# Performance work log

Hardware: AMD Instinct MI355X
Metric: run time of the kernel (lower is better)

The kernel has to match this reference:

```python
import jax, jax.numpy as jnp
import numpy as np

B, S, D, H = 4, 2048, 1024, 16
HD = D // H  # head_dim = 64


def setup_inputs() -> dict:
    key = jax.random.key(0)
    kx, kq, kk, kv, ko = jax.random.split(key, 5)
    scale = 1.0 / np.sqrt(D)
    return {
        "x": jax.random.normal(kx, (B, S, D), dtype=jnp.float32),
        "wq": jax.random.normal(kq, (D, D), dtype=jnp.float32) * scale,
        "wk": jax.random.normal(kk, (D, D), dtype=jnp.float32) * scale,
        "wv": jax.random.normal(kv, (D, D), dtype=jnp.float32) * scale,
        "wo": jax.random.normal(ko, (D, D), dtype=jnp.float32) * scale,
    }


def reference(x, wq, wk, wv, wo):
    b, s, d = x.shape
    # nn.Linear stores weight [out, in]: y = x @ W.T
    q = (x @ wq.T).reshape(b, s, H, HD)
    k = (x @ wk.T).reshape(b, s, H, HD)
    v = (x @ wv.T).reshape(b, s, H, HD)
    # scores: [b, h, s, s]
    scores = jnp.einsum("bqhd,bkhd->bhqk", q, k) / np.sqrt(HD)
    causal = jnp.triu(jnp.ones((s, s), dtype=bool), k=1)
    scores = jnp.where(causal, -jnp.inf, scores)
    attn = jax.nn.softmax(scores, axis=-1)
    out = jnp.einsum("bhqk,bkhd->bqhd", attn, v).reshape(b, s, d)
    return out @ wo.T
```

## Files before the change

### kernel.cpp

```cpp
#include <hip/hip_runtime.h>
#include <math.h>

typedef unsigned short u16;
typedef __attribute__((ext_vector_type(8))) short short8;
typedef __attribute__((ext_vector_type(4))) short short4v;
typedef __attribute__((ext_vector_type(4))) float f32x4;
typedef __attribute__((ext_vector_type(2))) unsigned int uint2v;
typedef __attribute__((ext_vector_type(4))) unsigned int uint4v;

constexpr int Bn = 4, Sn = 2048, Dn = 1024, Hn = 16;
constexpr float SCL = 0.125f * 1.44269504f;

__device__ __forceinline__ u16 f2bf(float f) {
  unsigned u = __float_as_uint(f);
  u += 0x7fffu + ((u >> 16) & 1u);
  return (u16)(u >> 16);
}

__device__ __forceinline__ f32x4 mfma32(short8 a, short8 b, f32x4 c) {
  return __builtin_amdgcn_mfma_f32_16x16x32_bf16(a, b, c, 0, 0, 0);
}

__device__ __forceinline__ void gl_lds16(const u16* g, u16* l) {
  __builtin_amdgcn_global_load_lds(
      (const __attribute__((address_space(1))) unsigned int*)g,
      (__attribute__((address_space(3))) unsigned int*)l, 16, 0, 0);
}

__global__ __launch_bounds__(256) void cast_all(
    const float4* __restrict__ x, const float4* __restrict__ wq,
    const float4* __restrict__ wk, const float4* __restrict__ wv,
    const float4* __restrict__ wo, ushort4* __restrict__ xb,
    ushort4* __restrict__ wqb, ushort4* __restrict__ wkb,
    ushort4* __restrict__ wvb, ushort4* __restrict__ wob) {
  const int blk = blockIdx.x;
  const float4* in;
  ushort4* out;
  int base;
  float s = 1.0f;
  if (blk < 8192) {
    in = x; out = xb; base = blk;
  } else if (blk < 9216) {
    in = wq; out = wqb; base = blk - 8192; s = SCL;
  } else if (blk < 10240) {
    in = wk; out = wkb; base = blk - 9216;
  } else if (blk < 11264) {
    in = wv; out = wvb; base = blk - 10240;
  } else {
    in = wo; out = wob; base = blk - 11264;
  }
  const int i = base * 256 + threadIdx.x;
  const float4 f = in[i];
  ushort4 o;
  o.x = f2bf(f.x * s); o.y = f2bf(f.y * s);
  o.z = f2bf(f.z * s); o.w = f2bf(f.w * s);
  out[i] = o;
}

template <int MODE>
__device__ __forceinline__ void gemm_body(const u16* __restrict__ A,
                                          const u16* __restrict__ W,
                                          u16* __restrict__ Cb,
                                          float* __restrict__ Cf,
                                          int bx, int by,
                                          u16* __restrict__ Asm,
                                          u16* __restrict__ Wsm) {
  const int t = threadIdx.x;
  const int w = t >> 6, l = t & 63;
  const int wy = w >> 1, wx = w & 1;
  const int q = l >> 4, r = l & 15;
  const int m0 = bx * 128, n0 = by * 128;

  f32x4 acc[4][4] = {};

  for (int k0 = 0; k0 < 1024; k0 += 64) {
    __syncthreads();
#pragma unroll
    for (int i = 0; i < 4; ++i) {
      const int c = t + i * 256;
      const int row = c >> 3, cl = c & 7;
      const int cg = cl ^ (row & 7);
      gl_lds16(A + (size_t)(m0 + row) * 1024 + k0 + cg * 8, &Asm[c * 8]);
      gl_lds16(W + (size_t)(n0 + row) * 1024 + k0 + cg * 8, &Wsm[c * 8]);
    }
    __syncthreads();
#pragma unroll
    for (int kf = 0; kf < 2; ++kf) {
      short8 af[4], bf[4];
#pragma unroll
      for (int mi = 0; mi < 4; ++mi) {
        const int rowA = wy * 64 + mi * 16 + r;
        af[mi] = *(const short8*)&Asm[rowA * 64 + ((kf * 4 + q) ^ (rowA & 7)) * 8];
        const int rowB = wx * 64 + mi * 16 + r;
        bf[mi] = *(const short8*)&Wsm[rowB * 64 + ((kf * 4 + q) ^ (rowB & 7)) * 8];
      }
#pragma unroll
      for (int mi = 0; mi < 4; ++mi)
#pragma unroll
        for (int ni = 0; ni < 4; ++ni)
          acc[mi][ni] = mfma32(af[mi], bf[ni], acc[mi][ni]);
    }
  }

  if (MODE == 2) {
    const int bq = m0 >> 11;
    const int jt = ((m0 & 2047) >> 6) + wy;
    const int hh = (n0 >> 6) + wx;
    u16* vt_t = Cb + ((size_t)((bq * 16 + hh) * 32) + jt) * 4096;
#pragma unroll
    for (int mi = 0; mi < 4; ++mi)
#pragma unroll
      for (int ni = 0; ni < 4; ++ni) {
        short4v pk;
#pragma unroll
        for (int e = 0; e < 4; ++e) pk[e] = (short)f2bf(acc[mi][ni][e]);
        const int hd = ni * 16 + r;
        const int c2 = q + 4 * (mi >> 1);
        *(short4v*)&vt_t[hd * 64 + ((c2 ^ (r & 7)) * 8) + (mi & 1) * 4] = pk;
      }
    return;
  }

#pragma unroll
  for (int mi = 0; mi < 4; ++mi) {
    const int row = m0 + wy * 64 + mi * 16 + q * 4;
#pragma unroll
    for (int ni = 0; ni < 4; ++ni) {
      const int col = n0 + wx * 64 + ni * 16 + r;
#pragma unroll
      for (int e = 0; e < 4; ++e) {
        if (MODE == 1)
          Cf[(size_t)(row + e) * 1024 + col] = acc[mi][ni][e];
        else
          Cb[(size_t)(row + e) * 1024 + col] = f2bf(acc[mi][ni][e]);
      }
    }
  }
}

__global__ __launch_bounds__(256) void gemm_qkv(const u16* __restrict__ A,
                                                const u16* __restrict__ Wq,
                                                const u16* __restrict__ Wk,
                                                const u16* __restrict__ Wv,
                                                u16* __restrict__ Cq,
                                                u16* __restrict__ Ck,
                                                u16* __restrict__ Vt) {
  __shared__ u16 Asm[128 * 64];
  __shared__ u16 Wsm[128 * 64];
  const int z = blockIdx.z;
  if (z == 2)
    gemm_body<2>(A, Wv, Vt, nullptr, blockIdx.x, blockIdx.y, Asm, Wsm);
  else
    gemm_body<0>(A, z ? Wk : Wq, z ? Ck : Cq, nullptr, blockIdx.x, blockIdx.y,
                 Asm, Wsm);
}

__global__ __launch_bounds__(256) void gemm_out(const u16* __restrict__ A,
                                                const u16* __restrict__ W,
                                                float* __restrict__ C) {
  __shared__ u16 Asm[128 * 64];
  __shared__ u16 Wsm[128 * 64];
  gemm_body<1>(A, W, nullptr, C, blockIdx.x, blockIdx.y, Asm, Wsm);
}

__global__ __launch_bounds__(128) void attn_v10(const u16* __restrict__ Qb,
                                                const u16* __restrict__ Kb,
                                                const u16* __restrict__ Vt,
                                                u16* __restrict__ Ob) {
  const int i = blockIdx.x;
  const int st = 31 - (i >> 6);
  const int grp = (i & 7) + 8 * ((i >> 3) & 7);
  const int b = grp >> 4, h = grp & 15;
  const int t = threadIdx.x;
  const int w = t >> 6, l = t & 63;
  const int q = l >> 4, r = l & 15;

  __shared__ u16 Kd[2][4096];
  __shared__ u16 Vd[4096];

  const size_t kgbase = (size_t)(b * Sn) * Dn + h * 64;
  const size_t vgbase = (size_t)((b * Hn + h) * 32) * 4096;

  const u16* kg[4];
  const u16* vg[4];
#pragma unroll
  for (int ii = 0; ii < 4; ++ii) {
    const int c = t + ii * 128, row = c >> 3, cl = c & 7;
    kg[ii] = Kb + kgbase + (size_t)row * Dn + (cl ^ (row & 7)) * 8;
    vg[ii] = Vt + vgbase + c * 8;
  }
  const int rx = r & 7;
  const int b0 = r * 64 + ((q ^ rx) * 8);
  const int b1 = r * 64 + (((4 + q) ^ rx) * 8);

  const int qb64 = st * 64;

  short8 Qf[2][2];
#pragma unroll
  for (int mi = 0; mi < 2; ++mi)
#pragma unroll
    for (int kf = 0; kf < 2; ++kf)
      Qf[mi][kf] = *(const short8*)(Qb +
          (size_t)(b * Sn + qb64 + w * 32 + mi * 16 + r) * Dn + h * 64 +
          kf * 32 + q * 8);

  f32x4 O[2][4] = {};
  float l_[2] = {0.f, 0.f};

#pragma unroll
  for (int ii = 0; ii < 4; ++ii)
    gl_lds16(kg[ii], &Kd[0][(t + ii * 128) * 8]);

  const u16* kgt[4];
  const u16* vgt[4];
#pragma unroll
  for (int ii = 0; ii < 4; ++ii) {
    kgt[ii] = kg[ii] + 64 * Dn;
    vgt[ii] = vg[ii];
  }

  for (int jt = 0; jt <= st; ++jt) {
    __syncthreads();

#pragma unroll
    for (int ii = 0; ii < 4; ++ii) {
      gl_lds16(vgt[ii], &Vd[(t + ii * 128) * 8]);
      vgt[ii] += 4096;
    }
    if (jt < st) {
      u16* kl = &Kd[(jt + 1) & 1][0];
#pragma unroll
      for (int ii = 0; ii < 4; ++ii) {
        gl_lds16(kgt[ii], kl + (t + ii * 128) * 8);
        kgt[ii] += 64 * Dn;
      }
    }

    const u16* KtA = &Kd[jt & 1][b0];
    const u16* KtB = &Kd[jt & 1][b1];

    short8 Kf[4][2];
#pragma unroll
    for (int ni = 0; ni < 4; ++ni) {
      Kf[ni][0] = *(const short8*)(KtA + ni * 1024);
      Kf[ni][1] = *(const short8*)(KtB + ni * 1024);
    }

    f32x4 S[2][4] = {};
    __builtin_amdgcn_s_setprio(1);
#pragma unroll
    for (int ni = 0; ni < 4; ++ni)
#pragma unroll
      for (int kf = 0; kf < 2; ++kf) {
        S[0][ni] = mfma32(Kf[ni][kf], Qf[0][kf], S[0][ni]);
        S[1][ni] = mfma32(Kf[ni][kf], Qf[1][kf], S[1][ni]);
      }
    __builtin_amdgcn_s_setprio(0);

    if (jt == st) {
#pragma unroll
      for (int mi = 0; mi < 2; ++mi) {
        const int qrow = w * 32 + mi * 16 + r;
#pragma unroll
        for (int ni = 0; ni < 4; ++ni) {
          const int key = ni * 16 + q * 4;
#pragma unroll
          for (int e = 0; e < 4; ++e)
            if (key + e > qrow) S[mi][ni][e] = -3.0e38f;
        }
      }
    }

    short8 P8[2][2];
#pragma unroll
    for (int mi = 0; mi < 2; ++mi)
#pragma unroll
      for (int np = 0; np < 2; ++np) {
        unsigned pw[4];
#pragma unroll
        for (int half = 0; half < 2; ++half) {
          const int ni = 2 * np + half;
          const float p0 = __builtin_amdgcn_exp2f(S[mi][ni][0]);
          const float p1 = __builtin_amdgcn_exp2f(S[mi][ni][1]);
          const float p2 = __builtin_amdgcn_exp2f(S[mi][ni][2]);
          const float p3 = __builtin_amdgcn_exp2f(S[mi][ni][3]);
          l_[mi] += (p0 + p1) + (p2 + p3);
          unsigned plo, phi;
          asm("v_cvt_pk_bf16_f32 %0, %1, %2" : "=v"(plo) : "v"(p0), "v"(p1));
          asm("v_cvt_pk_bf16_f32 %0, %1, %2" : "=v"(phi) : "v"(p2), "v"(p3));
          pw[half * 2] = plo;
          pw[half * 2 + 1] = phi;
        }
        const uint4v pk4 = {pw[0], pw[1], pw[2], pw[3]};
        P8[mi][np] = __builtin_bit_cast(short8, pk4);
      }

    if (jt < st)
      asm volatile("s_waitcnt vmcnt(4)" ::: "memory");
    else
      asm volatile("s_waitcnt vmcnt(0)" ::: "memory");
    __builtin_amdgcn_s_barrier();
    __builtin_amdgcn_sched_barrier(0);

    __builtin_amdgcn_s_setprio(1);
#pragma unroll
    for (int np = 0; np < 2; ++np) {
      const int vb = np ? b1 : b0;
#pragma unroll
      for (int ni2 = 0; ni2 < 4; ++ni2) {
        const short8 vvx = *(const short8*)(&Vd[vb + ni2 * 1024]);
        O[0][ni2] = mfma32(vvx, P8[0][np], O[0][ni2]);
        O[1][ni2] = mfma32(vvx, P8[1][np], O[1][ni2]);
      }
    }
    __builtin_amdgcn_s_setprio(0);
  }

#pragma unroll
  for (int mi = 0; mi < 2; ++mi) {
    float s = l_[mi];
    s += __shfl_xor(s, 16, 64);
    s += __shfl_xor(s, 32, 64);
    const float rl = __builtin_amdgcn_rcpf(s);
#pragma unroll
    for (int ni2 = 0; ni2 < 4; ++ni2) {
      short4v o;
#pragma unroll
      for (int e = 0; e < 4; ++e) o[e] = (short)f2bf(O[mi][ni2][e] * rl);
      *(short4v*)(Ob + (size_t)(b * Sn + qb64 + w * 32 + mi * 16 + r) * Dn +
                  h * 64 + ni2 * 16 + q * 4) = o;
    }
  }
}

extern "C" void kernel_launch(void* const* d_in, const int* in_sizes, int n_in,
                              void* d_out, int out_size, void* d_ws, size_t ws_size,
                              hipStream_t stream) {
  const float* x  = (const float*)d_in[0];
  const float* wq = (const float*)d_in[1];
  const float* wk = (const float*)d_in[2];
  const float* wv = (const float*)d_in[3];
  const float* wo = (const float*)d_in[4];
  float* out = (float*)d_out;

  u16* xb  = (u16*)d_ws;
  u16* wqb = xb + 8388608;
  u16* wkb = wqb + 1048576;
  u16* wvb = wkb + 1048576;
  u16* wob = wvb + 1048576;
  u16* qb  = wob + 1048576;
  u16* kb  = qb + 8388608;
  u16* vt2 = kb + 8388608;
  u16* aob = vt2 + 8388608;

  cast_all<<<12288, 256, 0, stream>>>(
      (const float4*)x, (const float4*)wq, (const float4*)wk,
      (const float4*)wv, (const float4*)wo, (ushort4*)xb, (ushort4*)wqb,
      (ushort4*)wkb, (ushort4*)wvb, (ushort4*)wob);

  gemm_qkv<<<dim3(64, 8, 3), 256, 0, stream>>>(xb, wqb, wkb, wvb, qb, kb, vt2);

  attn_v10<<<2048, 128, 0, stream>>>(qb, kb, vt2, aob);

  gemm_out<<<dim3(64, 8), 256, 0, stream>>>(aob, wob, out);
}
```

Before: 220.4 us.

## Rewrite QKV GEMM as 256x256 eight-wave kernel with pipelined LDS loads

Replaces the 128x128 four-wave QKV projection GEMM with a 256x256 tile, 512-thread kernel that double-buffers A/W tiles in 128KB LDS. Global-to-LDS loads are interleaved with quarter-tile MFMA phases, using explicit barriers, vmcnt waits and s_setprio around the compute. The aim is to raise data reuse per tile and hide memory latency behind MFMA work. In exchange, the grid shrinks to 384 blocks, which risks wave-quantization imbalance across CUs, and the hand-placed barriers and waitcnts are fragile. The out-projection GEMM is split into its own standalone kernel with unchanged logic.

```diff
diff --git a/kernel.cpp b/kernel.cpp
--- a/kernel.cpp
+++ b/kernel.cpp
@@ -26,6 +26,30 @@
       (const __attribute__((address_space(1))) unsigned int*)g,
       (__attribute__((address_space(3))) unsigned int*)l, 16, 0, 0);
 }
+
+#define BAR_IN()                                          \
+  do {                                                    \
+    __builtin_amdgcn_sched_barrier(0);                    \
+    __builtin_amdgcn_s_barrier();                         \
+    asm volatile("s_waitcnt lgkmcnt(0)" ::: "memory");    \
+    __builtin_amdgcn_sched_barrier(0);                    \
+    __builtin_amdgcn_s_setprio(1);                        \
+  } while (0)
+#define BAR_OUT()                                         \
+  do {                                                    \
+    __builtin_amdgcn_s_setprio(0);                        \
+    __builtin_amdgcn_sched_barrier(0);                    \
+    __builtin_amdgcn_s_barrier();                         \
+    __builtin_amdgcn_sched_barrier(0);                    \
+  } while (0)
+#define BAR_OUT_VM(N)                                     \
+  do {                                                    \
+    __builtin_amdgcn_s_setprio(0);                        \
+    __builtin_amdgcn_sched_barrier(0);                    \
+    asm volatile("s_waitcnt vmcnt(" #N ")" ::: "memory"); \
+    __builtin_amdgcn_s_barrier();                         \
+    __builtin_amdgcn_sched_barrier(0);                    \
+  } while (0)
 
 __global__ __launch_bounds__(256) void cast_all(
     const float4* __restrict__ x, const float4* __restrict__ wq,
@@ -57,19 +81,162 @@
   out[i] = o;
 }
 
-template <int MODE>
-__device__ __forceinline__ void gemm_body(const u16* __restrict__ A,
-                                          const u16* __restrict__ W,
-                                          u16* __restrict__ Cb,
-                                          float* __restrict__ Cf,
-                                          int bx, int by,
-                                          u16* __restrict__ Asm,
-                                          u16* __restrict__ Wsm) {
+__global__ __launch_bounds__(512, 2) void gemm_qkv8(
+    const u16* __restrict__ A, const u16* __restrict__ Wq,
+    const u16* __restrict__ Wk, const u16* __restrict__ Wv,
+    u16* __restrict__ Cq, u16* __restrict__ Ck, u16* __restrict__ Vt) {
+  __shared__ u16 lds[65536];
+
+  const int t = threadIdx.x;
+  const int w8 = t >> 6, l = t & 63;
+  const int wr = w8 >> 2, wc = w8 & 3;
+  const int q = l >> 4, r = l & 15;
+  const int m0 = blockIdx.x * 256, n0 = blockIdx.y * 256;
+  const int z = blockIdx.z;
+  const u16* __restrict__ W = z == 0 ? Wq : z == 1 ? Wk : Wv;
+
+  const u16* asrc[2];
+  const u16* wsrc[2];
+#pragma unroll
+  for (int ii = 0; ii < 2; ++ii) {
+    const int c = t + ii * 512, lr = c >> 3, cl = c & 7;
+    const int cg = cl ^ (lr & 7);
+    const int rowA0 = ((lr >> 6) << 7) + (lr & 63);
+    const int rowB0 = ((lr >> 5) << 6) + (lr & 31);
+    asrc[ii] = A + (size_t)(m0 + rowA0) * 1024 + cg * 8;
+    wsrc[ii] = W + (size_t)(n0 + rowB0) * 1024 + cg * 8;
+  }
+  const int dl0 = t * 8;
+
+  auto STA = [&](int kt, int ha) {
+#pragma unroll
+    for (int ii = 0; ii < 2; ++ii)
+      gl_lds16(asrc[ii] + ha * 65536 + kt * 64,
+               &lds[(kt & 1) * 16384 + ha * 8192 + dl0 + ii * 4096]);
+  };
+  auto STB = [&](int kt, int ha) {
+#pragma unroll
+    for (int ii = 0; ii < 2; ++ii)
+      gl_lds16(wsrc[ii] + ha * 32768 + kt * 64,
+               &lds[32768 + (kt & 1) * 16384 + ha * 8192 + dl0 + ii * 4096]);
+  };
+
+  f32x4 acc[8][4] = {};
+  short8 Af[4][2];
+  short8 Bf[2][2][2];
+
+  auto LDA = [&](int bufbase, int grp) {
+#pragma unroll
+    for (int m2 = 0; m2 < 4; ++m2) {
+      const int lro = bufbase + grp * 8192 + (wr * 64 + m2 * 16 + r) * 64;
+#pragma unroll
+      for (int kf = 0; kf < 2; ++kf)
+        Af[m2][kf] = *(const short8*)&lds[lro + (((kf * 4 + q) ^ (r & 7)) * 8)];
+    }
+  };
+  auto LDB = [&](int bufbase, int grp) {
+#pragma unroll
+    for (int n2 = 0; n2 < 2; ++n2) {
+      const int lro = bufbase + grp * 8192 + (wc * 32 + n2 * 16 + r) * 64;
+#pragma unroll
+      for (int kf = 0; kf < 2; ++kf)
+        Bf[grp][n2][kf] =
+            *(const short8*)&lds[lro + (((kf * 4 + q) ^ (r & 7)) * 8)];
+    }
+  };
+  auto MM = [&](int ag, int bg) {
+#pragma unroll
+    for (int kf = 0; kf < 2; ++kf)
+#pragma unroll
+      for (int m2 = 0; m2 < 4; ++m2)
+#pragma unroll
+        for (int n2 = 0; n2 < 2; ++n2)
+          acc[ag * 4 + m2][bg * 2 + n2] =
+              mfma32(Af[m2][kf], Bf[bg][n2][kf], acc[ag * 4 + m2][bg * 2 + n2]);
+  };
+
+  STA(0, 0); STB(0, 0); STA(0, 1); STB(0, 1);
+  STA(1, 0); STB(1, 0); STA(1, 1);
+  asm volatile("s_waitcnt vmcnt(6)" ::: "memory");
+  __builtin_amdgcn_s_barrier();
+  __builtin_amdgcn_sched_barrier(0);
+
+#pragma unroll 1
+  for (int i = 0; i < 8; ++i) {
+    const int kc = 2 * i;
+    const bool full = (i < 7);
+    LDA(0, 0); LDB(32768, 0);
+    STB(kc + 1, 1);
+    BAR_IN(); MM(0, 0); BAR_OUT();
+    LDB(32768, 1);
+    if (full) STA(kc + 2, 0);
+    BAR_IN(); MM(0, 1); BAR_OUT();
+    LDA(0, 1);
+    if (full) STB(kc + 2, 0);
+    BAR_IN(); MM(1, 1); BAR_OUT();
+    if (full) STA(kc + 2, 1);
+    BAR_IN(); MM(1, 0);
+    if (full) { BAR_OUT_VM(6); } else { BAR_OUT_VM(0); }
+    LDA(16384, 0); LDB(49152, 0);
+    if (full) STB(kc + 2, 1);
+    BAR_IN(); MM(0, 0); BAR_OUT();
+    LDB(49152, 1);
+    if (full) STA(kc + 3, 0);
+    BAR_IN(); MM(0, 1); BAR_OUT();
+    LDA(16384, 1);
+    if (full) STB(kc + 3, 0);
+    BAR_IN(); MM(1, 1); BAR_OUT();
+    if (full) {
+      STA(kc + 3, 1);
+      BAR_IN(); MM(1, 0); BAR_OUT_VM(6);
+    } else {
+      BAR_IN(); MM(1, 0); BAR_OUT();
+    }
+  }
+
+  if (z == 2) {
+    const int bq = m0 >> 11;
+    const int hh = (n0 >> 6) + wc;
+#pragma unroll
+    for (int mi = 0; mi < 8; ++mi) {
+      const int jt = ((m0 & 2047) >> 6) + wr * 2 + (mi >> 2);
+      const int m3 = mi & 3;
+      u16* vt_t = Vt + ((size_t)((bq * 16 + hh) * 32) + jt) * 4096;
+      const int slot = (((q + 4 * (m3 >> 1)) ^ (r & 7)) * 8) + (m3 & 1) * 4;
+#pragma unroll
+      for (int ni = 0; ni < 4; ++ni) {
+        short4v pk;
+#pragma unroll
+        for (int e = 0; e < 4; ++e) pk[e] = (short)f2bf(acc[mi][ni][e]);
+        *(short4v*)&vt_t[(ni * 16 + r) * 64 + slot] = pk;
+      }
+    }
+  } else {
+    u16* __restrict__ Cb = z ? Ck : Cq;
+#pragma unroll
+    for (int mi = 0; mi < 8; ++mi) {
+      const int row = m0 + wr * 128 + mi * 16 + q * 4;
+#pragma unroll
+      for (int ni = 0; ni < 4; ++ni) {
+        const int col = n0 + wc * 64 + ni * 16 + r;
+#pragma unroll
+        for (int e = 0; e < 4; ++e)
+          Cb[(size_t)(row + e) * 1024 + col] = f2bf(acc[mi][ni][e]);
+      }
+    }
+  }
+}
+
+__global__ __launch_bounds__(256) void gemm_out(const u16* __restrict__ A,
+                                                const u16* __restrict__ W,
+                                                float* __restrict__ C) {
+  __shared__ u16 Asm[128 * 64];
+  __shared__ u16 Wsm[128 * 64];
   const int t = threadIdx.x;
   const int w = t >> 6, l = t & 63;
   const int wy = w >> 1, wx = w & 1;
   const int q = l >> 4, r = l & 15;
-  const int m0 = bx * 128, n0 = by * 128;
+  const int m0 = blockIdx.x * 128, n0 = blockIdx.y * 128;
 
   f32x4 acc[4][4] = {};
 
@@ -102,25 +269,6 @@
     }
   }
 
-  if (MODE == 2) {
-    const int bq = m0 >> 11;
-    const int jt = ((m0 & 2047) >> 6) + wy;
-    const int hh = (n0 >> 6) + wx;
-    u16* vt_t = Cb + ((size_t)((bq * 16 + hh) * 32) + jt) * 4096;
-#pragma unroll
-    for (int mi = 0; mi < 4; ++mi)
-#pragma unroll
-      for (int ni = 0; ni < 4; ++ni) {
-        short4v pk;
-#pragma unroll
-        for (int e = 0; e < 4; ++e) pk[e] = (short)f2bf(acc[mi][ni][e]);
-        const int hd = ni * 16 + r;
-        const int c2 = q + 4 * (mi >> 1);
-        *(short4v*)&vt_t[hd * 64 + ((c2 ^ (r & 7)) * 8) + (mi & 1) * 4] = pk;
-      }
-    return;
-  }
-
 #pragma unroll
   for (int mi = 0; mi < 4; ++mi) {
     const int row = m0 + wy * 64 + mi * 16 + q * 4;
@@ -128,39 +276,10 @@
     for (int ni = 0; ni < 4; ++ni) {
       const int col = n0 + wx * 64 + ni * 16 + r;
 #pragma unroll
-      for (int e = 0; e < 4; ++e) {
-        if (MODE == 1)
-          Cf[(size_t)(row + e) * 1024 + col] = acc[mi][ni][e];
-        else
-          Cb[(size_t)(row + e) * 1024 + col] = f2bf(acc[mi][ni][e]);
-      }
-    }
-  }
-}
-
-__global__ __launch_bounds__(256) void gemm_qkv(const u16* __restrict__ A,
-                                                const u16* __restrict__ Wq,
-                                                const u16* __restrict__ Wk,
-                                                const u16* __restrict__ Wv,
-                                                u16* __restrict__ Cq,
-                                                u16* __restrict__ Ck,
-                                                u16* __restrict__ Vt) {
-  __shared__ u16 Asm[128 * 64];
-  __shared__ u16 Wsm[128 * 64];
-  const int z = blockIdx.z;
-  if (z == 2)
-    gemm_body<2>(A, Wv, Vt, nullptr, blockIdx.x, blockIdx.y, Asm, Wsm);
-  else
-    gemm_body<0>(A, z ? Wk : Wq, z ? Ck : Cq, nullptr, blockIdx.x, blockIdx.y,
-                 Asm, Wsm);
-}
-
-__global__ __launch_bounds__(256) void gemm_out(const u16* __restrict__ A,
-                                                const u16* __restrict__ W,
-                                                float* __restrict__ C) {
-  __shared__ u16 Asm[128 * 64];
-  __shared__ u16 Wsm[128 * 64];
-  gemm_body<1>(A, W, nullptr, C, blockIdx.x, blockIdx.y, Asm, Wsm);
+      for (int e = 0; e < 4; ++e)
+        C[(size_t)(row + e) * 1024 + col] = acc[mi][ni][e];
+    }
+  }
 }
 
 __global__ __launch_bounds__(128) void attn_v10(const u16* __restrict__ Qb,
@@ -358,7 +477,7 @@
       (const float4*)wv, (const float4*)wo, (ushort4*)xb, (ushort4*)wqb,
       (ushort4*)wkb, (ushort4*)wvb, (ushort4*)wob);
 
-  gemm_qkv<<<dim3(64, 8, 3), 256, 0, stream>>>(xb, wqb, wkb, wvb, qb, kb, vt2);
+  gemm_qkv8<<<dim3(32, 4, 3), 512, 0, stream>>>(xb, wqb, wkb, wvb, qb, kb, vt2);
 
   attn_v10<<<2048, 128, 0, stream>>>(qb, kb, vt2, aob);
 
```

Measured after the change: 232.2 us. 5.4% more time.
